# Performance work log

Measured on AMD Instinct MI355X. Metric: run time of the kernel, lower is better.

Reference implementation:

```python
import jax, jax.numpy as jnp
import numpy as np
from jax import lax

EPS = 1e-7  # keras backend epsilon used by K.ctc_batch_cost
NEG = -1e30  # log-space 'zero'


def setup_inputs() -> dict:
    key = jax.random.key(0)
    k1, k2 = jax.random.split(key)
    B, T, C, L = 512, 512, 128, 48
    # softmax-like probabilities over classes (ctc_batch_cost expects probs)
    u = jax.random.uniform(k1, (B, T, C), dtype=jnp.float32, minval=1e-3, maxval=1.0)
    y_pred = u / jnp.sum(u, axis=-1, keepdims=True)
    # labels in [0, C-2]; blank index is C-1 (keras convention)
    y_true = jax.random.randint(k2, (B, L), 0, C - 1, dtype=jnp.int64)
    return {"y_true": y_true, "y_pred": y_pred}


def _ctc_loss(y_true, y_pred):
    # y_true: [B, L] int labels; y_pred: [B, T, C] probabilities
    B, T, C = y_pred.shape
    L = y_true.shape[1]
    S = 2 * L + 1
    blank = C - 1

    log_probs = jnp.log(y_pred + EPS)  # [B, T, C]

    # extended label sequence: blank, l1, blank, l2, ..., blank -> [B, S]
    ext = jnp.full((B, S), blank, dtype=y_true.dtype).at[:, 1::2].set(y_true)
    ext_m2 = jnp.concatenate(
        [jnp.full((B, 2), -1, dtype=ext.dtype), ext[:, :-2]], axis=1
    )
    # skip-transition allowed iff current symbol is a non-blank differing from s-2
    skip = (ext != blank) & (ext != ext_m2)  # [B, S]

    # gather per-extended-symbol log probs: [B, T, S] -> time-major [T, B, S]
    lp_ext = jnp.take_along_axis(log_probs, ext[:, None, :], axis=2)
    lp_ext = jnp.moveaxis(lp_ext, 1, 0)

    neg = jnp.asarray(NEG, log_probs.dtype)
    alpha0 = jnp.full((B, S), neg)
    alpha0 = alpha0.at[:, 0].set(lp_ext[0, :, 0]).at[:, 1].set(lp_ext[0, :, 1])

    def step(alpha, lp_t):
        a1 = alpha
        a2 = jnp.concatenate([jnp.full((B, 1), neg), alpha[:, :-1]], axis=1)
        a3 = jnp.concatenate([jnp.full((B, 2), neg), alpha[:, :-2]], axis=1)
        a3 = jnp.where(skip, a3, neg)
        new = jnp.logaddexp(jnp.logaddexp(a1, a2), a3) + lp_t
        return new, None

    alpha_T, _ = lax.scan(step, alpha0, lp_ext[1:])
    # total log-likelihood ends in last blank or last label
    loglik = jnp.logaddexp(alpha_T[:, -1], alpha_T[:, -2])
    return -loglik[:, None]  # [B, 1] like K.ctc_batch_cost


def reference(y_true, y_pred):
    return _ctc_loss(y_true, y_pred)
```

## Files before the change

### kernel.cpp

```cpp
#include <hip/hip_runtime.h>


constexpr int Bc = 512, Tc = 512, Cc = 128, Lc = 48;
constexpr float FEPS = 1e-7f;
constexpr float FNEG = -1e30f;
constexpr float LN2F = 0.69314718055994530942f;
constexpr int CDEAD = -(1 << 28);

#define DPP_WAVE_SHR1 0x138
#define DPP_WAVE_SHL1 0x130

__device__ __forceinline__ float dppf_shr1(float x) {
    return __int_as_float(__builtin_amdgcn_update_dpp(
        0, __float_as_int(x), DPP_WAVE_SHR1, 0xF, 0xF, false));
}
__device__ __forceinline__ float dppf_shl1(float x) {
    return __int_as_float(__builtin_amdgcn_update_dpp(
        0, __float_as_int(x), DPP_WAVE_SHL1, 0xF, 0xF, false));
}
__device__ __forceinline__ int dppi_shr1_self(int c) {
    return __builtin_amdgcn_update_dpp(c, c, DPP_WAVE_SHR1, 0xF, 0xF, false);
}
__device__ __forceinline__ int dppi_shl1_self(int c) {
    return __builtin_amdgcn_update_dpp(c, c, DPP_WAVE_SHL1, 0xF, 0xF, false);
}

__device__ __forceinline__ float lae2(float a, float b) {
    float m = fmaxf(a, b);
    float d = fabsf(a - b);
    return m + __log2f(1.0f + __builtin_amdgcn_exp2f(-d));
}
__device__ __forceinline__ float rd63f(float v) {
    return __uint_as_float((unsigned)
        __builtin_amdgcn_readlane(__float_as_uint(v), 63));
}

__global__ __launch_bounds__(128)
void ctc_fb_kernel(const int* __restrict__ y_true,
                   const float* __restrict__ y_pred,
                   float* __restrict__ out) {
    const int b = blockIdx.x;
    const int lane = threadIdx.x & 63;
    const int wave = threadIdx.x >> 6;

    const float* yb = y_pred + (size_t)b * Tc * Cc;

    const int lab = (lane < Lc) ? y_true[b * Lc + lane] : (Cc - 1);
    const int labm1 = __builtin_amdgcn_ds_bpermute(((lane + 63) & 63) << 2, lab);
    const bool skip  = (lab != (Cc - 1)) && (lab != labm1);
    const bool validhi = (lane < Lc);
    const bool lane0 = (lane == 0);

    __shared__ float sblo[64], sbhi[64];
    __shared__ int sbc[64];

    float lo = 0.0f, hi = 0.0f;
    int c = CDEAD;

    auto renorm = [&]() {
        float mx = fmaxf(lo, hi);
        int e = (int)((__float_as_uint(mx) >> 23) & 0xFF) - 127;
        e = (mx > 0.0f) ? e : 0;
        lo = ldexpf(lo, -e);
        hi = ldexpf(hi, -e);
        c += e;
    };

    float p0[16], p1[16], p2[16], p3[16];
    float pbf[16], phf[16];

    auto batchv = [&](float (&pr)[16]) {
        #pragma unroll
        for (int j = 0; j < 16; ++j) {
            pbf[j] = rd63f(pr[j]) + FEPS;
            phf[j] = validhi ? (pr[j] + FEPS) : 0.0f;
        }
    };

    if (wave == 0) {
        auto step = [&](int j) {
            float sh  = dppf_shr1(hi);
            int   cm1 = dppi_shr1_self(c);
            bool  own_dead = (lo == 0.0f) && (hi == 0.0f);
            int   m  = own_dead ? cm1 : ((c > cm1) ? c : cm1);
            float lov = ldexpf(lo, c - m);
            float hiv = ldexpf(hi, c - m);
            float shv = ldexpf(sh, cm1 - m);
            float a3  = skip ? shv : 0.0f;
            lo = (lov + shv) * pbf[j];
            hi = (hiv + lov + a3) * phf[j];
            c = m;
        };
        auto steps16 = [&]() {
            #pragma unroll
            for (int j = 0; j < 16; ++j) {
                step(j);
                if (j == 7 || j == 15) renorm();
            }
        };
        auto issue = [&](float (&buf)[16], int g) {
            const float* base = yb + (size_t)(g * 16) * Cc + lab;
            #pragma unroll
            for (int j = 0; j < 16; ++j) buf[j] = base[(size_t)j * Cc];
        };
        issue(p0, 0); issue(p1, 1); issue(p2, 2); issue(p3, 3);
        batchv(p0); issue(p0, 4);
        lo = lane0 ? pbf[0] : 0.0f;
        hi = lane0 ? phf[0] : 0.0f;
        c  = lane0 ? 0 : CDEAD;
        #pragma unroll
        for (int j = 1; j < 16; ++j) {
            step(j);
            if (j == 7 || j == 15) renorm();
        }
        batchv(p1); issue(p1, 5); steps16();
        batchv(p2); issue(p2, 6); steps16();
        batchv(p3); issue(p3, 7); steps16();
        #pragma unroll 1
        for (int G = 1; G < 4; ++G) {
            const int g = 4 * G;
            batchv(p0); if (g + 4 < 16) issue(p0, g + 4); steps16();
            batchv(p1); if (g + 5 < 16) issue(p1, g + 5); steps16();
            batchv(p2); if (g + 6 < 16) issue(p2, g + 6); steps16();
            batchv(p3); if (g + 7 < 16) issue(p3, g + 7); steps16();
        }
    } else {
        auto step = [&](int j) {
            float qlo = lo * pbf[j];
            float qhi = hi * phf[j];
            float u   = qlo + (skip ? qhi : 0.0f);
            float un  = dppf_shl1(u);
            int   cp1 = dppi_shl1_self(c);
            bool  own_dead = (qlo == 0.0f) && (qhi == 0.0f);
            int   m  = own_dead ? cp1 : ((c > cp1) ? c : cp1);
            lo = ldexpf(qlo + qhi, c - m);
            hi = ldexpf(qhi, c - m) + ldexpf(un, cp1 - m);
            c = m;
        };
        auto steps16 = [&]() {
            #pragma unroll
            for (int j = 0; j < 16; ++j) {
                step(j);
                if (j == 7 || j == 15) renorm();
            }
        };
        auto issue = [&](float (&buf)[16], int g) {
            const int t0 = 511 - g * 16;
            const float* base = yb + lab;
            #pragma unroll
            for (int j = 0; j < 16; ++j) buf[j] = base[(size_t)(t0 - j) * Cc];
        };
        lo = (lane == 48) ? 1.0f : 0.0f;
        hi = (lane == 47) ? 1.0f : 0.0f;
        c  = (lane == 47 || lane == 48) ? 0 : CDEAD;
        issue(p0, 0); issue(p1, 1); issue(p2, 2); issue(p3, 3);
        batchv(p0); issue(p0, 4); steps16();
        batchv(p1); issue(p1, 5); steps16();
        batchv(p2); issue(p2, 6); steps16();
        batchv(p3); issue(p3, 7); steps16();
        #pragma unroll 1
        for (int G = 1; G < 4; ++G) {
            const int g = 4 * G;
            batchv(p0); if (g + 4 < 16) issue(p0, g + 4); steps16();
            batchv(p1); if (g + 5 < 16) issue(p1, g + 5); steps16();
            batchv(p2); if (g + 6 < 16) issue(p2, g + 6); steps16();
            batchv(p3); if (g + 7 < 16) issue(p3, g + 7); steps16();
        }
        sblo[lane] = lo;
        sbhi[lane] = hi;
        sbc[lane]  = c;
    }

    __syncthreads();

    if (wave == 0) {
        float blo = sblo[lane], bhi = sbhi[lane];
        float ctot = (float)(c + sbc[lane]);
        float plo = lo * blo;
        float phi = hi * bhi;
        float yl = (plo > 0.0f) ? (__log2f(plo) + ctot) : FNEG;
        float yh = (phi > 0.0f) ? (__log2f(phi) + ctot) : FNEG;
        float v = lae2(yl, yh);
        #pragma unroll
        for (int mk = 1; mk < 64; mk <<= 1)
            v = lae2(v, __shfl_xor(v, mk, 64));
        if (lane0) out[b] = -(v * LN2F);
    }
}

extern "C" void kernel_launch(void* const* d_in, const int* in_sizes, int n_in,
                              void* d_out, int out_size, void* d_ws, size_t ws_size,
                              hipStream_t stream) {
    const int* y_true = (const int*)d_in[0];
    const float* y_pred = (const float*)d_in[1];
    float* out = (float*)d_out;
    hipLaunchKernelGGL(ctc_fb_kernel, dim3(Bc), dim3(128), 0, stream,
                       y_true, y_pred, out);
}
```

Baseline: 34.36 us.

## Load full class rows coalesced as float2 and gather labels via ds_bpermute

Each lane now loads a contiguous float2 slice of the 128-class row for every timestep instead of a scattered per-label element. The per-label probabilities are then picked out in registers with cross-lane ds_bpermute and an odd/even select. The blank probability comes from a readlane of lane 63's second element. Prefetch depth drops from four 16-step buffers to two, which trades scattered gather loads for coalesced loads plus extra LDS permute instructions, with less latency hiding.

```diff
diff --git a/kernel.cpp b/kernel.cpp
--- a/kernel.cpp
+++ b/kernel.cpp
@@ -24,7 +24,6 @@
 __device__ __forceinline__ int dppi_shl1_self(int c) {
     return __builtin_amdgcn_update_dpp(c, c, DPP_WAVE_SHL1, 0xF, 0xF, false);
 }
-
 __device__ __forceinline__ float lae2(float a, float b) {
     float m = fmaxf(a, b);
     float d = fabsf(a - b);
@@ -33,6 +32,9 @@
 __device__ __forceinline__ float rd63f(float v) {
     return __uint_as_float((unsigned)
         __builtin_amdgcn_readlane(__float_as_uint(v), 63));
+}
+__device__ __forceinline__ float bperm_f(int byteaddr, float v) {
+    return __int_as_float(__builtin_amdgcn_ds_bpermute(byteaddr, __float_as_int(v)));
 }
 
 __global__ __launch_bounds__(128)
@@ -50,6 +52,8 @@
     const bool skip  = (lab != (Cc - 1)) && (lab != labm1);
     const bool validhi = (lane < Lc);
     const bool lane0 = (lane == 0);
+    const int rowaddr = (lab >> 1) << 2;
+    const bool odd = (lab & 1) != 0;
 
     __shared__ float sblo[64], sbhi[64];
     __shared__ int sbc[64];
@@ -66,14 +70,17 @@
         c += e;
     };
 
-    float p0[16], p1[16], p2[16], p3[16];
+    float2 rA[16], rB[16];
     float pbf[16], phf[16];
 
-    auto batchv = [&](float (&pr)[16]) {
+    auto batch = [&](float2 (&buf)[16]) {
         #pragma unroll
         for (int j = 0; j < 16; ++j) {
-            pbf[j] = rd63f(pr[j]) + FEPS;
-            phf[j] = validhi ? (pr[j] + FEPS) : 0.0f;
+            float v0 = bperm_f(rowaddr, buf[j].x);
+            float v1 = bperm_f(rowaddr, buf[j].y);
+            float praw = odd ? v1 : v0;
+            pbf[j] = rd63f(buf[j].y) + FEPS;
+            phf[j] = validhi ? (praw + FEPS) : 0.0f;
         }
     };
 
@@ -98,13 +105,14 @@
                 if (j == 7 || j == 15) renorm();
             }
         };
-        auto issue = [&](float (&buf)[16], int g) {
-            const float* base = yb + (size_t)(g * 16) * Cc + lab;
+        auto issue = [&](float2 (&buf)[16], int g) {
+            const float* base = yb + (size_t)(g * 16) * Cc + lane * 2;
             #pragma unroll
-            for (int j = 0; j < 16; ++j) buf[j] = base[(size_t)j * Cc];
+            for (int j = 0; j < 16; ++j)
+                buf[j] = *reinterpret_cast<const float2*>(base + (size_t)j * Cc);
         };
-        issue(p0, 0); issue(p1, 1); issue(p2, 2); issue(p3, 3);
-        batchv(p0); issue(p0, 4);
+        issue(rA, 0); issue(rB, 1);
+        batch(rA); issue(rA, 2);
         lo = lane0 ? pbf[0] : 0.0f;
         hi = lane0 ? phf[0] : 0.0f;
         c  = lane0 ? 0 : CDEAD;
@@ -113,16 +121,11 @@
             step(j);
             if (j == 7 || j == 15) renorm();
         }
-        batchv(p1); issue(p1, 5); steps16();
-        batchv(p2); issue(p2, 6); steps16();
-        batchv(p3); issue(p3, 7); steps16();
+        batch(rB); issue(rB, 3); steps16();
         #pragma unroll 1
-        for (int G = 1; G < 4; ++G) {
-            const int g = 4 * G;
-            batchv(p0); if (g + 4 < 16) issue(p0, g + 4); steps16();
-            batchv(p1); if (g + 5 < 16) issue(p1, g + 5); steps16();
-            batchv(p2); if (g + 6 < 16) issue(p2, g + 6); steps16();
-            batchv(p3); if (g + 7 < 16) issue(p3, g + 7); steps16();
+        for (int k = 1; k < 8; ++k) {
+            batch(rA); if (2 * k + 2 < 16) issue(rA, 2 * k + 2); steps16();
+            batch(rB); if (2 * k + 3 < 16) issue(rB, 2 * k + 3); steps16();
         }
     } else {
         auto step = [&](int j) {
@@ -144,27 +147,23 @@
                 if (j == 7 || j == 15) renorm();
             }
         };
-        auto issue = [&](float (&buf)[16], int g) {
+        auto issue = [&](float2 (&buf)[16], int g) {
             const int t0 = 511 - g * 16;
-            const float* base = yb + lab;
+            const float* base = yb + lane * 2;
             #pragma unroll
-            for (int j = 0; j < 16; ++j) buf[j] = base[(size_t)(t0 - j) * Cc];
+            for (int j = 0; j < 16; ++j)
+                buf[j] = *reinterpret_cast<const float2*>(base + (size_t)(t0 - j) * Cc);
         };
         lo = (lane == 48) ? 1.0f : 0.0f;
         hi = (lane == 47) ? 1.0f : 0.0f;
         c  = (lane == 47 || lane == 48) ? 0 : CDEAD;
-        issue(p0, 0); issue(p1, 1); issue(p2, 2); issue(p3, 3);
-        batchv(p0); issue(p0, 4); steps16();
-        batchv(p1); issue(p1, 5); steps16();
-        batchv(p2); issue(p2, 6); steps16();
-        batchv(p3); issue(p3, 7); steps16();
+        issue(rA, 0); issue(rB, 1);
+        batch(rA); issue(rA, 2); steps16();
+        batch(rB); issue(rB, 3); steps16();
         #pragma unroll 1
-        for (int G = 1; G < 4; ++G) {
-            const int g = 4 * G;
-            batchv(p0); if (g + 4 < 16) issue(p0, g + 4); steps16();
-            batchv(p1); if (g + 5 < 16) issue(p1, g + 5); steps16();
-            batchv(p2); if (g + 6 < 16) issue(p2, g + 6); steps16();
-            batchv(p3); if (g + 7 < 16) issue(p3, g + 7); steps16();
+        for (int k = 1; k < 8; ++k) {
+            batch(rA); if (2 * k + 2 < 16) issue(rA, 2 * k + 2); steps16();
+            batch(rB); if (2 * k + 3 < 16) issue(rB, 2 * k + 3); steps16();
         }
         sblo[lane] = lo;
         sbhi[lane] = hi;
```

Measured after the change: 32.48 us. 5.5% less time.
